# Optimization experiments

Hardware: AMD Instinct MI355X
Metric: run time of the kernel (lower is better)

## Reference

```python
import jax, jax.numpy as jnp
import numpy as np

B, T, HID = 8, 2048, 1024
NH, MD = 16, 16
UFC = 2  # len(use_for_context) = ['lr', 'rl']
MAT_EPS = 1e-5
VEC_EPS = 1e-6
SQRT_MD = float(np.sqrt(MD))


def setup_inputs() -> dict:
    key = jax.random.key(0)
    ks = jax.random.split(key, 5)
    s_in = 1.0 / np.sqrt(HID)
    s_out = 1.0 / np.sqrt(NH * MD * UFC)
    return {
        "hidden_states": jax.random.normal(ks[0], (B, T, HID), jnp.float32),
        "W_mat": jax.random.uniform(ks[1], (HID, NH * MD * MD), jnp.float32, -s_in, s_in),
        "b_mat": jax.random.uniform(ks[2], (NH * MD * MD,), jnp.float32, -s_in, s_in),
        "W_out": jax.random.uniform(ks[3], (NH * MD * UFC, HID), jnp.float32, -s_out, s_out),
        "b_out": jax.random.uniform(ks[4], (HID,), jnp.float32, -s_out, s_out),
    }


def _scan_vectors(m, v0, reverse):
    """Sequential matrix-vector recurrence with per-step L2 normalization.
    m: (T, B*NH, d, d); v0: (B*NH, d). Returns history (T, B*NH, d)
    (equal to torch history[1:] for lr, and reversed(history[1:]) for rl)."""
    def step(v, m_t):
        nv = jnp.einsum('bij,bj->bi', m_t, v)
        nv = nv / (jnp.linalg.norm(nv, axis=-1, keepdims=True) + VEC_EPS)
        return nv, nv
    _, hist = jax.lax.scan(step, v0, m, reverse=reverse)
    return hist


def reference(hidden_states, W_mat, b_mat, W_out, b_out):
    # predict_matrix: fc_to_mat + Frobenius matrix normalization ([-2,-1] branch)
    m = hidden_states @ W_mat + b_mat                       # (B, T, NH*MD*MD)
    m = m.reshape(B, T, NH, MD, MD).transpose(1, 0, 2, 3, 4)  # (T, B, NH, d, d)
    fro = jnp.linalg.norm(m, axis=(-2, -1), keepdims=True)
    m_norm = m / (fro + MAT_EPS) * SQRT_MD
    m_norm = m_norm.reshape(T, B * NH, MD, MD)

    # init_type == 'one': v[..., 0, :] = 1 -> e_0
    v0 = jnp.zeros((B * NH, MD), jnp.float32).at[:, 0].set(1.0)

    v_lr = _scan_vectors(m_norm, v0, reverse=False)  # (T, B*NH, d)
    v_rl = _scan_vectors(m_norm, v0, reverse=True)   # (T, B*NH, d)

    def to_bthd(v):
        return v.reshape(T, B, NH, MD).transpose(1, 0, 2, 3)  # (B, T, NH, d)

    x = jnp.concatenate([to_bthd(v_lr), to_bthd(v_rl)], axis=-1)  # (B, T, NH, 2d)
    # networks_for_heads == 'common': flatten heads, Linear, gelu (exact erf form)
    x = x.reshape(B, T, NH * MD * UFC) @ W_out + b_out
    return jax.nn.gelu(x, approximate=False)
```

## Files before the change

kernel.cpp:

```cpp
#include <hip/hip_runtime.h>
#include <math.h>

#define Tdim 2048
#define HIDd 1024
#define NHd 16
#define NCOL 4096
#define Cn 64
#define Ln 32
#define LSTR 40
#define KCAT 3072
#define KB 6144

typedef _Float16 f16x4  __attribute__((ext_vector_type(4)));
typedef _Float16 f16x8  __attribute__((ext_vector_type(8)));
typedef float    f32x4  __attribute__((ext_vector_type(4)));

typedef __attribute__((address_space(1))) void gvoid_t;
typedef __attribute__((address_space(3))) void lvoid_t;

__global__ __launch_bounds__(256) void conv_A_kernel(const float* __restrict__ hs,
                                                     _Float16* __restrict__ Ac)
{
    const size_t i = ((size_t)blockIdx.x * 256 + threadIdx.x) * 8;
    const size_t r = i >> 10, k = i & 1023;
    const float4 x0 = *(const float4*)(hs + i);
    const float4 x1 = *(const float4*)(hs + i + 4);
    const float v[8] = {x0.x, x0.y, x0.z, x0.w, x1.x, x1.y, x1.z, x1.w};
    f16x8 h, hm, l;
#pragma unroll
    for (int j = 0; j < 8; ++j) {
        const _Float16 hh = (_Float16)v[j];
        h[j]  = hh;
        hm[j] = (_Float16)(v[j] * 0.03125f);
        l[j]  = (_Float16)((v[j] - (float)hh) * 32.0f);
    }
    _Float16* o = Ac + r * KCAT + k;
    *(f16x8*)(o)        = h;
    *(f16x8*)(o + 1024) = hm;
    *(f16x8*)(o + 2048) = l;
}

__global__ __launch_bounds__(256) void conv_B_kernel(const float* __restrict__ W,
                                                     _Float16* __restrict__ Bc)
{
    __shared__ float t[32][33];
    const int tx = threadIdx.x & 31, ty = threadIdx.x >> 5;
    const int n0 = blockIdx.x * 32, k0 = blockIdx.y * 32;
#pragma unroll
    for (int i = 0; i < 4; ++i)
        t[ty + i * 8][tx] = W[(size_t)(k0 + ty + i * 8) * NCOL + n0 + tx];
    __syncthreads();
#pragma unroll
    for (int i = 0; i < 4; ++i) {
        const float w = t[tx][ty + i * 8];
        const _Float16 h = (_Float16)w;
        const size_t o = (size_t)(n0 + ty + i * 8) * KCAT + k0 + tx;
        Bc[o]        = h;
        Bc[o + 1024] = (_Float16)((w - (float)h) * 32.0f);
        Bc[o + 2048] = (_Float16)((float)h * 0.03125f);
    }
}

__global__ __launch_bounds__(256) void conv_W2T_kernel(const float* __restrict__ W,
                                                       _Float16* __restrict__ WT)
{
    __shared__ float t[32][33];
    const int tx = threadIdx.x & 31, ty = threadIdx.x >> 5;
    const int n0 = blockIdx.x * 32, k0 = blockIdx.y * 32;
#pragma unroll
    for (int i = 0; i < 4; ++i)
        t[ty + i * 8][tx] = W[(size_t)(k0 + ty + i * 8) * 1024 + n0 + tx];
    __syncthreads();
#pragma unroll
    for (int i = 0; i < 4; ++i)
        WT[(size_t)(n0 + ty + i * 8) * 512 + k0 + tx] = (_Float16)t[tx][ty + i * 8];
}

#define MFMA_PHASE(CPH) \
    _Pragma("unroll") \
    for (int m2_ = 0; m2_ < 2; ++m2_) { \
        _Pragma("unroll") \
        for (int nt_ = 0; nt_ < 4; ++nt_) { \
            acc[(CPH)*2 + m2_][nt_] = __builtin_amdgcn_mfma_f32_16x16x32_f16(af[m2_][0], bf[nt_][0], acc[(CPH)*2 + m2_][nt_], 0, 0, 0); \
            acc[(CPH)*2 + m2_][nt_] = __builtin_amdgcn_mfma_f32_16x16x32_f16(af[m2_][1], bf[nt_][1], acc[(CPH)*2 + m2_][nt_], 0, 0, 0); \
        } \
    }

#define PHASE(BUF, CPH, STAGE_EXPR, DOGATE) do { \
    af[0][0] = readA(BUF, (CPH)*2,     0); \
    af[0][1] = readA(BUF, (CPH)*2,     1); \
    af[1][0] = readA(BUF, (CPH)*2 + 1, 0); \
    af[1][1] = readA(BUF, (CPH)*2 + 1, 1); \
    if ((CPH) == 0) { \
        _Pragma("unroll") \
        for (int nt_ = 0; nt_ < 4; ++nt_) { bf[nt_][0] = readB(BUF, nt_, 0); bf[nt_][1] = readB(BUF, nt_, 1); } \
    } \
    STAGE_EXPR; \
    asm volatile("s_barrier" ::: "memory"); \
    asm volatile("s_waitcnt lgkmcnt(0)" ::: "memory"); \
    __builtin_amdgcn_sched_barrier(0); \
    __builtin_amdgcn_s_setprio(1); \
    MFMA_PHASE(CPH) \
    __builtin_amdgcn_s_setprio(0); \
    if (DOGATE) { \
        if (notlast) asm volatile("s_waitcnt vmcnt(6)" ::: "memory"); \
        else         asm volatile("s_waitcnt vmcnt(0)" ::: "memory"); \
    } \
    asm volatile("s_barrier" ::: "memory"); \
} while (0)

__global__ __launch_bounds__(512, 2) void gemm1_8ph(const _Float16* __restrict__ A,
                                                    const _Float16* __restrict__ B,
                                                    const float* __restrict__ bias,
                                                    float* __restrict__ Mout)
{
    __shared__ __align__(16) _Float16 sA[2][256 * 64];
    __shared__ __align__(16) _Float16 sB[2][256 * 64];
    const int tid = threadIdx.x;
    const int lane = tid & 63;
    const int wid = tid >> 6;
    const int wm = wid >> 2, wn = wid & 3;
    const int q = lane >> 4, ln = lane & 15;
    const int col0 = blockIdx.x * 256;
    const int row0 = blockIdx.y * 256;

    const char* Ab = (const char*)A + (size_t)row0 * KB;
    const char* Bb = (const char*)B + (size_t)col0 * KB;

    auto stage_chunk = [&](const char* g, int fr, int kt, char* ldsbase) {
        const int rr = tid >> 3;
        const int cb = (tid & 7) << 4;
        const char* src = g + (size_t)(fr + rr) * KB + (size_t)kt * 128 + (cb ^ ((rr & 7) << 4));
        char* dst = ldsbase + ((tid >> 6) << 10);
        __builtin_amdgcn_global_load_lds((gvoid_t*)src, (lvoid_t*)dst, 16, 0, 0);
    };
    auto stageA2 = [&](int b, int t, int h) {
        stage_chunk(Ab, h * 64,       t, (char*)&sA[b][0] + (size_t)(h * 64) * 128);
        stage_chunk(Ab, 128 + h * 64, t, (char*)&sA[b][0] + (size_t)(128 + h * 64) * 128);
    };
    auto stageB2 = [&](int b, int t, int h) {
        stage_chunk(Bb, h * 128,      t, (char*)&sB[b][0] + (size_t)(h * 128) * 128);
        stage_chunk(Bb, h * 128 + 64, t, (char*)&sB[b][0] + (size_t)(h * 128 + 64) * 128);
    };
    auto readA = [&](int b, int mf, int ks) -> f16x8 {
        const int r = wm * 128 + mf * 16 + ln;
        return *(const f16x8*)((const char*)&sA[b][0] + r * 128 + ((ks * 64 + q * 16) ^ ((r & 7) << 4)));
    };
    auto readB = [&](int b, int nt, int ks) -> f16x8 {
        const int r = wn * 64 + nt * 16 + ln;
        return *(const f16x8*)((const char*)&sB[b][0] + r * 128 + ((ks * 64 + q * 16) ^ ((r & 7) << 4)));
    };

    stageB2(0, 0, 0); stageB2(0, 0, 1); stageA2(0, 0, 0); stageA2(0, 0, 1);
    stageB2(1, 1, 0); stageB2(1, 1, 1); stageA2(1, 1, 0);

    f32x4 acc[8][4];
    const f32x4 z4 = {0.f, 0.f, 0.f, 0.f};
#pragma unroll
    for (int mf = 0; mf < 8; ++mf)
#pragma unroll
        for (int nt = 0; nt < 4; ++nt) acc[mf][nt] = z4;

    asm volatile("s_waitcnt vmcnt(6)" ::: "memory");
    asm volatile("s_barrier" ::: "memory");

    f16x8 af[2][2];
    f16x8 bf[4][2];

#pragma unroll 1
    for (int it = 0; it < 24; ++it) {
        const int t0 = it * 2;
        const bool notlast = (it != 23);
        PHASE(0, 0, (stageA2(1, t0 + 1, 1)), 0);
        PHASE(0, 1, (notlast ? stageB2(0, t0 + 2, 0) : (void)0), 0);
        PHASE(0, 2, (notlast ? stageB2(0, t0 + 2, 1) : (void)0), 0);
        PHASE(0, 3, (notlast ? stageA2(0, t0 + 2, 0) : (void)0), 1);
        PHASE(1, 0, (notlast ? stageA2(0, t0 + 2, 1) : (void)0), 0);
        PHASE(1, 1, (notlast ? stageB2(1, t0 + 3, 0) : (void)0), 0);
        PHASE(1, 2, (notlast ? stageB2(1, t0 + 3, 1) : (void)0), 0);
        PHASE(1, 3, (notlast ? stageA2(1, t0 + 3, 0) : (void)0), 1);
    }

#pragma unroll
    for (int nt = 0; nt < 4; ++nt) {
        const int c = col0 + wn * 64 + nt * 16 + ln;
        const float bv = bias[c];
        const int h = c >> 8, e = c & 255;
#pragma unroll
        for (int mf = 0; mf < 8; ++mf) {
#pragma unroll
            for (int r = 0; r < 4; ++r) {
                const int row = row0 + wm * 128 + mf * 16 + q * 4 + r;
                const int bbl = row >> 11, t = row & 2047;
                Mout[((size_t)(bbl * 16 + h) * Tdim + t) * 256 + e] = acc[mf][nt][r] + bv;
            }
        }
    }
}

__global__ __launch_bounds__(128) void stageA2_mfma(const float* __restrict__ m,
                                                    float* __restrict__ q,
                                                    _Float16* __restrict__ P, int SS)
{
    const int tid = threadIdx.x;
    const int dir = tid >> 6;
    const int lane = tid & 63;
    const int qd = lane >> 4, ln = lane & 15;
    const int sc = blockIdx.x;
    const int seq = sc >> 6, c = sc & (Cn - 1);
    const float* mp = m + ((size_t)seq * Tdim + c * Ln) * 256;
    _Float16* Pp = P + (((size_t)(dir * SS + seq) * Cn + c) * Ln) * 256
                     + (qd * 4) * 16 + ln;

    float v[4];
#pragma unroll
    for (int r = 0; r < 4; ++r) v[r] = (qd * 4 + r == ln) ? 1.0f : 0.0f;

    const int dstep = dir ? -256 : 256;
    const float* Ms = mp + (dir ? (Ln - 1) * 256 : 0) + ln * 16 + qd * 4;

    float4 arow = *(const float4*)Ms;
    float f2 = arow.x*arow.x + arow.y*arow.y + arow.z*arow.z + arow.w*arow.w;
#pragma unroll
    for (int off = 1; off < 64; off <<= 1) f2 += __shfl_xor(f2, off);
    float sm = 4.0f * rsqrtf(f2 + 1e-12f);

    for (int s = 0; s < Ln; ++s) {
        f16x4 mh, mlo;
        const float ar[4] = {arow.x * sm, arow.y * sm, arow.z * sm, arow.w * sm};
#pragma unroll
        for (int i = 0; i < 4; ++i) {
            const _Float16 h = (_Float16)ar[i];
            mh[i] = h; mlo[i] = (_Float16)((ar[i] - (float)h) * 1024.0f);
        }
        float smn = sm;
        if (s + 1 < Ln) {
            Ms += dstep;
            arow = *(const float4*)Ms;
            float f2n = arow.x*arow.x + arow.y*arow.y + arow.z*arow.z + arow.w*arow.w;
#pragma unroll
            for (int off = 1; off < 64; off <<= 1) f2n += __shfl_xor(f2n, off);
            smn = 4.0f * rsqrtf(f2n + 1e-12f);
        }
        f16x4 qh, ql;
#pragma unroll
        for (int r = 0; r < 4; ++r) {
            const _Float16 h = (_Float16)v[r];
            qh[r] = h; ql[r] = (_Float16)((v[r] - (float)h) * 1024.0f);
        }
        f32x4 a1 = {0.f,0.f,0.f,0.f}, a2 = {0.f,0.f,0.f,0.f};
        a1 = __builtin_amdgcn_mfma_f32_16x16x16f16(mh,  qh, a1, 0, 0, 0);
        a2 = __builtin_amdgcn_mfma_f32_16x16x16f16(mh,  ql, a2, 0, 0, 0);
        a2 = __builtin_amdgcn_mfma_f32_16x16x16f16(mlo, qh, a2, 0, 0, 0);
#pragma unroll
        for (int r = 0; r < 4; ++r) v[r] = a1[r] + a2[r] * (1.0f / 1024.0f);

        if (s & 1) {
            float mx = 0.f;
#pragma unroll
            for (int r = 0; r < 4; ++r) mx = fmaxf(mx, fabsf(v[r]));
#pragma unroll
            for (int off = 1; off < 64; off <<= 1) mx = fmaxf(mx, __shfl_xor(mx, off));
            const float inv = 1.0f / (mx + 1e-30f);
#pragma unroll
            for (int r = 0; r < 4; ++r) v[r] *= inv;
        }
#pragma unroll
        for (int r = 0; r < 4; ++r)
            Pp[(size_t)s * 256 + r * 16] = (_Float16)v[r];
        sm = smn;
    }

    float ss = 0.f;
#pragma unroll
    for (int r = 0; r < 4; ++r) ss += v[r] * v[r];
#pragma unroll
    for (int off = 1; off < 64; off <<= 1) ss += __shfl_xor(ss, off);
    const float sl = 1.0f / (sqrtf(ss) + 1e-30f);
    float* qo = q + ((size_t)(dir * SS + seq) * Cn + c) * 256;
#pragma unroll
    for (int r = 0; r < 4; ++r)
        qo[(qd * 4 + r) * 16 + ln] = v[r] * sl;
}

__global__ __launch_bounds__(64) void stageB_kernel(const float* __restrict__ q,
                                                    float* __restrict__ vs, int SS)
{
    const int lane = threadIdx.x & 63;
    const int i = lane & 15;
    const int chain = blockIdx.x;
    const int dir = (chain >= SS) ? 1 : 0;
    const int seq = chain - dir * SS;
    const float* qb = q + (size_t)(dir * SS + seq) * Cn * 256;
    float* vb = vs + (size_t)(dir * SS + seq) * Cn * 16;

    float myw = (i == 0) ? 1.0f : 0.0f;
    float wv[16];
#pragma unroll
    for (int k2 = 0; k2 < 16; ++k2) wv[k2] = (k2 == 0) ? 1.0f : 0.0f;

    int cc = dir ? (Cn - 1) : 0;
    const float* Qp = qb + (size_t)cc * 256 + i * 16;
    float4 q0 = *(const float4*)(Qp + 0);
    float4 q1 = *(const float4*)(Qp + 4);
    float4 q2 = *(const float4*)(Qp + 8);
    float4 q3 = *(const float4*)(Qp + 12);

    for (int s = 0; s < Cn; ++s) {
        vb[cc * 16 + i] = myw;
        float nv = q0.x*wv[0] + q0.y*wv[1] + q0.z*wv[2] + q0.w*wv[3]
                 + q1.x*wv[4] + q1.y*wv[5] + q1.z*wv[6] + q1.w*wv[7]
                 + q2.x*wv[8] + q2.y*wv[9] + q2.z*wv[10] + q2.w*wv[11]
                 + q3.x*wv[12] + q3.y*wv[13] + q3.z*wv[14] + q3.w*wv[15];
        if (s + 1 < Cn) {
            const int ccn = dir ? (Cn - 2 - s) : (s + 1);
            const float* Qn = qb + (size_t)ccn * 256 + i * 16;
            q0 = *(const float4*)(Qn + 0);
            q1 = *(const float4*)(Qn + 4);
            q2 = *(const float4*)(Qn + 8);
            q3 = *(const float4*)(Qn + 12);
        }
        float s2 = nv * nv;
        s2 += __shfl_xor(s2, 1); s2 += __shfl_xor(s2, 2);
        s2 += __shfl_xor(s2, 4); s2 += __shfl_xor(s2, 8);
        const float wn = nv / (sqrtf(s2) + 1e-20f);
        myw = wn;
#pragma unroll
        for (int k2 = 0; k2 < 16; ++k2) wv[k2] = __shfl(wn, (lane & 48) | k2);
        cc = dir ? (Cn - 2 - s) : (s + 1);
    }
}

__global__ __launch_bounds__(256) void stageC2_kernel(const _Float16* __restrict__ P,
                                                      const float* __restrict__ vs,
                                                      _Float16* __restrict__ x, int SS)
{
    const int tid = threadIdx.x;
    const int wave = tid >> 6, lane = tid & 63;
    const int dsc = blockIdx.x * 4 + wave;
    const int dirseq = dsc >> 6, c = dsc & (Cn - 1);
    const int dir = (dirseq >= SS) ? 1 : 0;
    const int seq = dirseq - dir * SS;
    const int bbl = seq >> 4, h = seq & 15;
    const _Float16* Pp = P + (size_t)dsc * (Ln * 256);
    const float* vp = vs + (size_t)dsc * 16;

    float v[16];
#pragma unroll
    for (int k = 0; k < 16; ++k) v[k] = vp[k];

    const int tt = lane >> 4, j = lane & 15;
    const int t0 = c * Ln;
#pragma unroll
    for (int g = 0; g < 8; ++g) {
        const int s = g * 4 + tt;
        const _Float16* pr = Pp + (size_t)s * 256 + j * 16;
        const f16x8 p0 = *(const f16x8*)(pr);
        const f16x8 p1 = *(const f16x8*)(pr + 8);
        float nv = 0.f;
#pragma unroll
        for (int k = 0; k < 8; ++k) nv += (float)p0[k] * v[k];
#pragma unroll
        for (int k = 0; k < 8; ++k) nv += (float)p1[k] * v[k + 8];
        float s2 = nv * nv;
        s2 += __shfl_xor(s2, 1); s2 += __shfl_xor(s2, 2);
        s2 += __shfl_xor(s2, 4); s2 += __shfl_xor(s2, 8);
        const float vn = nv / (sqrtf(s2) + 1e-6f);
        const int t = dir ? (t0 + Ln - 1 - s) : (t0 + s);
        x[(((size_t)bbl * Tdim + t) * NHd + h) * 32 + dir * 16 + j] = (_Float16)vn;
    }
}

__global__ __launch_bounds__(256) void gemm2_f16(const _Float16* __restrict__ A,
                                                 const _Float16* __restrict__ BT,
                                                 const float* __restrict__ bias,
                                                 float* __restrict__ out, int row0)
{
    __shared__ _Float16 Al[128 * LSTR];
    __shared__ _Float16 Bl[128 * LSTR];
    const int tid = threadIdx.x;
    const int wave = tid >> 6, lane = tid & 63;
    const int wm = wave & 1, wn = wave >> 1;
    const int qd = lane >> 4, ln = lane & 15;
    const int r0 = blockIdx.y * 128;
    const int c0 = blockIdx.x * 128;

    f32x4 acc[4][4] = {{{0.f,0.f,0.f,0.f}}};

    const int sr = tid >> 2, sc = tid & 3;
    const _Float16* Ag = A  + (size_t)(r0 + sr) * 512 + sc * 8;
    const _Float16* Bg = BT + (size_t)(c0 + sr) * 512 + sc * 8;
    _Float16* Alw = &Al[sr * LSTR + sc * 8];
    _Float16* Blw = &Bl[sr * LSTR + sc * 8];

    for (int k0 = 0; k0 < 512; k0 += 32) {
        const f16x8 a0 = *(const f16x8*)(Ag + k0);
        const f16x8 a1 = *(const f16x8*)(Ag + (size_t)64 * 512 + k0);
        const f16x8 b0 = *(const f16x8*)(Bg + k0);
        const f16x8 b1 = *(const f16x8*)(Bg + (size_t)64 * 512 + k0);
        __syncthreads();
        *(f16x8*)(Alw)             = a0;
        *(f16x8*)(Alw + 64 * LSTR) = a1;
        *(f16x8*)(Blw)             = b0;
        *(f16x8*)(Blw + 64 * LSTR) = b1;
        __syncthreads();
        f16x8 af[4], bfr[4];
#pragma unroll
        for (int mt = 0; mt < 4; ++mt)
            af[mt] = *(const f16x8*)&Al[(wm * 64 + mt * 16 + ln) * LSTR + qd * 8];
#pragma unroll
        for (int nt = 0; nt < 4; ++nt)
            bfr[nt] = *(const f16x8*)&Bl[(wn * 64 + nt * 16 + ln) * LSTR + qd * 8];
#pragma unroll
        for (int mt = 0; mt < 4; ++mt)
#pragma unroll
            for (int nt = 0; nt < 4; ++nt)
                acc[mt][nt] = __builtin_amdgcn_mfma_f32_16x16x32_f16(af[mt], bfr[nt], acc[mt][nt], 0, 0, 0);
    }
#pragma unroll
    for (int nt = 0; nt < 4; ++nt) {
        const int c = c0 + wn * 64 + nt * 16 + ln;
        const float bv = bias[c];
#pragma unroll
        for (int mt = 0; mt < 4; ++mt) {
#pragma unroll
            for (int r = 0; r < 4; ++r) {
                const int row = r0 + wm * 64 + mt * 16 + qd * 4 + r;
                float v = acc[mt][nt][r] + bv;
                v = 0.5f * v * (1.0f + erff(v * 0.70710678118654752f));
                out[(size_t)(row0 + row) * 1024 + c] = v;
            }
        }
    }
}

extern "C" void kernel_launch(void* const* d_in, const int* in_sizes, int n_in,
                              void* d_out, int out_size, void* d_ws, size_t ws_size,
                              hipStream_t stream)
{
    const float* hs    = (const float*)d_in[0];
    const float* W_mat = (const float*)d_in[1];
    const float* b_mat = (const float*)d_in[2];
    const float* W_out = (const float*)d_in[3];
    const float* b_out = (const float*)d_in[4];
    float* out = (float*)d_out;

    const size_t per_bb = (32ull << 20) + (2ull << 20) + (12ull << 20) + (32ull << 20)
                        + (128ull << 10);
    const size_t wbase  = 25ull << 20;
    int nbb = 8;
    while (nbb > 1 && ws_size < wbase + (size_t)nbb * per_bb) nbb >>= 1;

    char* base = (char*)d_ws;
    _Float16* W2T = (_Float16*)base;
    _Float16* Bc  = (_Float16*)(base + (1ull << 20));
    size_t off = wbase;
    float* m  = (float*)(base + off);  off += (size_t)nbb * (32ull << 20);
    float* qx = (float*)(base + off);  off += (size_t)nbb * (2ull << 20);
    _Float16* Ac = (_Float16*)(base + off); off += (size_t)nbb * (12ull << 20);
    _Float16* P  = (_Float16*)(base + off); off += (size_t)nbb * (32ull << 20);
    float* vs = (float*)(base + off);

    conv_B_kernel<<<dim3(128, 32), 256, 0, stream>>>(W_mat, Bc);
    conv_W2T_kernel<<<dim3(32, 16), 256, 0, stream>>>(W_out, W2T);

    for (int bb0 = 0; bb0 < 8; bb0 += nbb) {
        const int row0 = bb0 * Tdim;
        const int SS = nbb * 16;
        conv_A_kernel<<<nbb * 1024, 256, 0, stream>>>(hs + (size_t)row0 * HIDd, Ac);
        gemm1_8ph<<<dim3(16, nbb * 8), 512, 0, stream>>>(Ac, Bc, b_mat, m);
        stageA2_mfma<<<SS * 64, 128, 0, stream>>>(m, qx, P, SS);
        stageB_kernel<<<2 * SS, 64, 0, stream>>>(qx, vs, SS);
        stageC2_kernel<<<SS * 32, 256, 0, stream>>>(P, vs, (_Float16*)qx, SS);
        gemm2_f16<<<dim3(8, nbb * 16), 256, 0, stream>>>((_Float16*)qx, W2T, b_out, out, row0);
    }
}
```

Baseline: 941.6 us.

## Store chunk products in place over the matrix buffer, dropping separate P buffer

stageA2 now copies its 32-step chunk of normalized matrices into LDS, then writes the fp16 prefix products back into the same global region of m, split into two half-rows by direction. stageC2 reads the products from m at the new stride with time-ordered indexing. This drops the separate 32MB-per-batch P buffer, cutting memory footprint and write traffic and possibly letting more batches run per launch. In exchange it adds an LDS staging copy and relies on the in-place overwrite being race-free within each block.

```diff
diff --git a/kernel.cpp b/kernel.cpp
--- a/kernel.cpp
+++ b/kernel.cpp
@@ -134,7 +134,7 @@
         char* dst = ldsbase + ((tid >> 6) << 10);
         __builtin_amdgcn_global_load_lds((gvoid_t*)src, (lvoid_t*)dst, 16, 0, 0);
     };
-    auto stageA2 = [&](int b, int t, int h) {
+    auto stageA2g = [&](int b, int t, int h) {
         stage_chunk(Ab, h * 64,       t, (char*)&sA[b][0] + (size_t)(h * 64) * 128);
         stage_chunk(Ab, 128 + h * 64, t, (char*)&sA[b][0] + (size_t)(128 + h * 64) * 128);
     };
@@ -151,8 +151,8 @@
         return *(const f16x8*)((const char*)&sB[b][0] + r * 128 + ((ks * 64 + q * 16) ^ ((r & 7) << 4)));
     };
 
-    stageB2(0, 0, 0); stageB2(0, 0, 1); stageA2(0, 0, 0); stageA2(0, 0, 1);
-    stageB2(1, 1, 0); stageB2(1, 1, 1); stageA2(1, 1, 0);
+    stageB2(0, 0, 0); stageB2(0, 0, 1); stageA2g(0, 0, 0); stageA2g(0, 0, 1);
+    stageB2(1, 1, 0); stageB2(1, 1, 1); stageA2g(1, 1, 0);
 
     f32x4 acc[8][4];
     const f32x4 z4 = {0.f, 0.f, 0.f, 0.f};
@@ -171,14 +171,14 @@
     for (int it = 0; it < 24; ++it) {
         const int t0 = it * 2;
         const bool notlast = (it != 23);
-        PHASE(0, 0, (stageA2(1, t0 + 1, 1)), 0);
+        PHASE(0, 0, (stageA2g(1, t0 + 1, 1)), 0);
         PHASE(0, 1, (notlast ? stageB2(0, t0 + 2, 0) : (void)0), 0);
         PHASE(0, 2, (notlast ? stageB2(0, t0 + 2, 1) : (void)0), 0);
-        PHASE(0, 3, (notlast ? stageA2(0, t0 + 2, 0) : (void)0), 1);
-        PHASE(1, 0, (notlast ? stageA2(0, t0 + 2, 1) : (void)0), 0);
+        PHASE(0, 3, (notlast ? stageA2g(0, t0 + 2, 0) : (void)0), 1);
+        PHASE(1, 0, (notlast ? stageA2g(0, t0 + 2, 1) : (void)0), 0);
         PHASE(1, 1, (notlast ? stageB2(1, t0 + 3, 0) : (void)0), 0);
         PHASE(1, 2, (notlast ? stageB2(1, t0 + 3, 1) : (void)0), 0);
-        PHASE(1, 3, (notlast ? stageA2(1, t0 + 3, 0) : (void)0), 1);
+        PHASE(1, 3, (notlast ? stageA2g(1, t0 + 3, 0) : (void)0), 1);
     }
 
 #pragma unroll
@@ -198,34 +198,43 @@
     }
 }
 
-__global__ __launch_bounds__(128) void stageA2_mfma(const float* __restrict__ m,
-                                                    float* __restrict__ q,
-                                                    _Float16* __restrict__ P, int SS)
-{
+__global__ __launch_bounds__(128) void stageA2_mfma(float* __restrict__ m,
+                                                    float* __restrict__ q, int SS)
+{
+    __shared__ float Ml[Ln * 256];
     const int tid = threadIdx.x;
     const int dir = tid >> 6;
     const int lane = tid & 63;
     const int qd = lane >> 4, ln = lane & 15;
     const int sc = blockIdx.x;
     const int seq = sc >> 6, c = sc & (Cn - 1);
-    const float* mp = m + ((size_t)seq * Tdim + c * Ln) * 256;
-    _Float16* Pp = P + (((size_t)(dir * SS + seq) * Cn + c) * Ln) * 256
-                     + (qd * 4) * 16 + ln;
+    float* mp = m + ((size_t)seq * Tdim + c * Ln) * 256;
+
+    {
+        const float4* src = (const float4*)mp;
+        float4* dst = (float4*)Ml;
+#pragma unroll
+        for (int i = 0; i < 16; ++i)
+            dst[tid + i * 128] = src[tid + i * 128];
+    }
+    __syncthreads();
 
     float v[4];
 #pragma unroll
     for (int r = 0; r < 4; ++r) v[r] = (qd * 4 + r == ln) ? 1.0f : 0.0f;
 
-    const int dstep = dir ? -256 : 256;
-    const float* Ms = mp + (dir ? (Ln - 1) * 256 : 0) + ln * 16 + qd * 4;
-
-    float4 arow = *(const float4*)Ms;
+    const int s0 = dir ? (Ln - 1) : 0;
+    const int ds = dir ? -1 : 1;
+
+    int t = s0;
+    float4 arow = *(const float4*)&Ml[t * 256 + ln * 16 + qd * 4];
     float f2 = arow.x*arow.x + arow.y*arow.y + arow.z*arow.z + arow.w*arow.w;
 #pragma unroll
     for (int off = 1; off < 64; off <<= 1) f2 += __shfl_xor(f2, off);
     float sm = 4.0f * rsqrtf(f2 + 1e-12f);
 
     for (int s = 0; s < Ln; ++s) {
+        const int tcur = t;
         f16x4 mh, mlo;
         const float ar[4] = {arow.x * sm, arow.y * sm, arow.z * sm, arow.w * sm};
 #pragma unroll
@@ -235,8 +244,8 @@
         }
         float smn = sm;
         if (s + 1 < Ln) {
-            Ms += dstep;
-            arow = *(const float4*)Ms;
+            t += ds;
+            arow = *(const float4*)&Ml[t * 256 + ln * 16 + qd * 4];
             float f2n = arow.x*arow.x + arow.y*arow.y + arow.z*arow.z + arow.w*arow.w;
 #pragma unroll
             for (int off = 1; off < 64; off <<= 1) f2n += __shfl_xor(f2n, off);
@@ -265,9 +274,10 @@
 #pragma unroll
             for (int r = 0; r < 4; ++r) v[r] *= inv;
         }
+        _Float16* Pp = (_Float16*)((char*)mp + (size_t)tcur * 1024 + dir * 512);
 #pragma unroll
         for (int r = 0; r < 4; ++r)
-            Pp[(size_t)s * 256 + r * 16] = (_Float16)v[r];
+            Pp[(qd * 4 + r) * 16 + ln] = (_Float16)v[r];
         sm = smn;
     }
 
@@ -331,7 +341,7 @@
     }
 }
 
-__global__ __launch_bounds__(256) void stageC2_kernel(const _Float16* __restrict__ P,
+__global__ __launch_bounds__(256) void stageC2_kernel(const float* __restrict__ m,
                                                       const float* __restrict__ vs,
                                                       _Float16* __restrict__ x, int SS)
 {
@@ -342,7 +352,8 @@
     const int dir = (dirseq >= SS) ? 1 : 0;
     const int seq = dirseq - dir * SS;
     const int bbl = seq >> 4, h = seq & 15;
-    const _Float16* Pp = P + (size_t)dsc * (Ln * 256);
+    const _Float16* Pp = (const _Float16*)((const char*)m
+                       + ((size_t)seq * Tdim + c * Ln) * 1024 + dir * 512);
     const float* vp = vs + (size_t)dsc * 16;
 
     float v[16];
@@ -354,7 +365,7 @@
 #pragma unroll
     for (int g = 0; g < 8; ++g) {
         const int s = g * 4 + tt;
-        const _Float16* pr = Pp + (size_t)s * 256 + j * 16;
+        const _Float16* pr = Pp + (size_t)s * 512 + j * 16;
         const f16x8 p0 = *(const f16x8*)(pr);
         const f16x8 p1 = *(const f16x8*)(pr + 8);
         float nv = 0.f;
@@ -366,7 +377,7 @@
         s2 += __shfl_xor(s2, 1); s2 += __shfl_xor(s2, 2);
         s2 += __shfl_xor(s2, 4); s2 += __shfl_xor(s2, 8);
         const float vn = nv / (sqrtf(s2) + 1e-6f);
-        const int t = dir ? (t0 + Ln - 1 - s) : (t0 + s);
+        const int t = t0 + s;
         x[(((size_t)bbl * Tdim + t) * NHd + h) * 32 + dir * 16 + j] = (_Float16)vn;
     }
 }
@@ -445,8 +456,7 @@
     const float* b_out = (const float*)d_in[4];
     float* out = (float*)d_out;
 
-    const size_t per_bb = (32ull << 20) + (2ull << 20) + (12ull << 20) + (32ull << 20)
-                        + (128ull << 10);
+    const size_t per_bb = (32ull << 20) + (2ull << 20) + (12ull << 20) + (128ull << 10);
     const size_t wbase  = 25ull << 20;
     int nbb = 8;
     while (nbb > 1 && ws_size < wbase + (size_t)nbb * per_bb) nbb >>= 1;
@@ -458,7 +468,6 @@
     float* m  = (float*)(base + off);  off += (size_t)nbb * (32ull << 20);
     float* qx = (float*)(base + off);  off += (size_t)nbb * (2ull << 20);
     _Float16* Ac = (_Float16*)(base + off); off += (size_t)nbb * (12ull << 20);
-    _Float16* P  = (_Float16*)(base + off); off += (size_t)nbb * (32ull << 20);
     float* vs = (float*)(base + off);
 
     conv_B_kernel<<<dim3(128, 32), 256, 0, stream>>>(W_mat, Bc);
@@ -469,9 +478,9 @@
         const int SS = nbb * 16;
         conv_A_kernel<<<nbb * 1024, 256, 0, stream>>>(hs + (size_t)row0 * HIDd, Ac);
         gemm1_8ph<<<dim3(16, nbb * 8), 512, 0, stream>>>(Ac, Bc, b_mat, m);
-        stageA2_mfma<<<SS * 64, 128, 0, stream>>>(m, qx, P, SS);
+        stageA2_mfma<<<SS * Cn, 128, 0, stream>>>(m, qx, SS);
         stageB_kernel<<<2 * SS, 64, 0, stream>>>(qx, vs, SS);
-        stageC2_kernel<<<SS * 32, 256, 0, stream>>>(P, vs, (_Float16*)qx, SS);
+        stageC2_kernel<<<SS * Cn / 2, 256, 0, stream>>>(m, vs, (_Float16*)qx, SS);
         gemm2_f16<<<dim3(8, nbb * 16), 256, 0, stream>>>((_Float16*)qx, W2T, b_out, out, row0);
     }
 }
```

Result: faster. 877.9 us (-6.8%).
